# Optimization experiments

Hardware: AMD Instinct MI355X
Metric: run time of the kernel (lower is better)

The kernel has to match this reference:

```python
import jax, jax.numpy as jnp
import numpy as np

N_NODES = 100000
N_EDGES = 3200000
IN_CH = 256
OUT_CH = 1


def setup_inputs() -> dict:
    key = jax.random.key(0)
    ks = jax.random.split(key, 8)
    x = jax.random.normal(ks[0], (N_NODES, IN_CH), dtype=jnp.float32)
    edge_index = jax.random.randint(ks[1], (2, N_EDGES), 0, N_NODES, dtype=jnp.int64 if jax.config.jax_enable_x64 else jnp.int32)
    s_in = 1.0 / np.sqrt(IN_CH)
    Wq = jax.random.uniform(ks[2], (IN_CH, OUT_CH), jnp.float32, -s_in, s_in)
    bq = jax.random.uniform(ks[3], (OUT_CH,), jnp.float32, -s_in, s_in)
    Wk = jax.random.uniform(ks[4], (IN_CH, OUT_CH), jnp.float32, -s_in, s_in)
    bk = jax.random.uniform(ks[5], (OUT_CH,), jnp.float32, -s_in, s_in)
    Wv = jax.random.uniform(ks[6], (IN_CH, IN_CH), jnp.float32, -s_in, s_in)
    bv = jax.random.uniform(ks[7], (IN_CH,), jnp.float32, -s_in, s_in)
    return {"x": x, "edge_index": edge_index, "Wq": Wq, "bq": bq,
            "Wk": Wk, "bk": bk, "Wv": Wv, "bv": bv}


def reference(x, edge_index, Wq, bq, Wk, bk, Wv, bv):
    num_nodes = x.shape[0]
    q = x @ Wq + bq                       # [N, out_ch]
    k = x @ Wk + bk                       # [N, out_ch]
    v = x @ Wv + bv                       # [N, in_ch]
    row, col = edge_index[0], edge_index[1]
    # edge attention logits: gather + dot over out_ch
    att = jnp.sum(q[row] * k[col], axis=-1)          # [E]
    att = jax.nn.leaky_relu(att, negative_slope=0.2)
    att = jax.nn.softmax(att, axis=0)                # softmax over ALL edges (dim=0)
    # scatter-add edge attention to source nodes
    attention_weights = jax.ops.segment_sum(att, row, num_segments=num_nodes)  # [N]
    graph_emb = jnp.sum(attention_weights[:, None] * v, axis=0)                # [in_ch]
    return graph_emb, attention_weights
```

## Files before the change

kernel.cpp:

```cpp
#include <hip/hip_runtime.h>

#define N_NODES 100000
#define N_EDGES 3200000
#define CH 256

#define GRID_QK 1563
#define GRID_POOL 512
#define YCOPY 16

#define NR 8
#define RANGE 12500
#define SL 64
#define EPS 50000
#define HEPS 25000
#define GP 391

#define OFF_TOTAL 0
#define OFF_PTOT  16
#define OFF_YU16  528
#define OFF_Q     4624
#define OFF_K     104624
#define OFF_AWU   204624
#define OFF_PART  304624

__global__ __launch_bounds__(256) void k_qk(const float* __restrict__ x,
                                            const float* __restrict__ Wq,
                                            const float* __restrict__ bq,
                                            const float* __restrict__ Wk,
                                            const float* __restrict__ bk,
                                            float* __restrict__ q,
                                            float* __restrict__ k,
                                            float* __restrict__ yu16) {
    int t = threadIdx.x;
    if (blockIdx.x < 16) yu16[blockIdx.x * 256 + t] = 0.0f;
    int w = t >> 6, lane = t & 63;
    int g = lane >> 4, seg = lane & 15;
    float4 wq4[4], wk4[4];
    #pragma unroll
    for (int j = 0; j < 4; ++j) {
        wq4[j] = ((const float4*)Wq)[seg + 16 * j];
        wk4[j] = ((const float4*)Wk)[seg + 16 * j];
    }
    float bqs = bq[0], bks = bk[0];
    int base = blockIdx.x * 64 + w * 16 + g;
    #pragma unroll
    for (int i = 0; i < 4; ++i) {
        int n = base + i * 4;
        if (n < N_NODES) {
            const float4* xr = (const float4*)(x + (size_t)n * CH);
            float dq = 0.0f, dk = 0.0f;
            #pragma unroll
            for (int j = 0; j < 4; ++j) {
                float4 xv = xr[seg + 16 * j];
                dq = fmaf(xv.x, wq4[j].x, fmaf(xv.y, wq4[j].y,
                     fmaf(xv.z, wq4[j].z, fmaf(xv.w, wq4[j].w, dq))));
                dk = fmaf(xv.x, wk4[j].x, fmaf(xv.y, wk4[j].y,
                     fmaf(xv.z, wk4[j].z, fmaf(xv.w, wk4[j].w, dk))));
            }
            dq += __shfl_down(dq, 8); dq += __shfl_down(dq, 4);
            dq += __shfl_down(dq, 2); dq += __shfl_down(dq, 1);
            dk += __shfl_down(dk, 8); dk += __shfl_down(dk, 4);
            dk += __shfl_down(dk, 2); dk += __shfl_down(dk, 1);
            if (seg == 0) { q[n] = dq + bqs; k[n] = dk + bks; }
        }
    }
}

__global__ __launch_bounds__(1024) void k_acc(const int* __restrict__ ei,
                                              const float* __restrict__ q,
                                              const float* __restrict__ k,
                                              float* __restrict__ partial) {
    __shared__ float acc[RANGE];
    int t = threadIdx.x;
    int s = blockIdx.x >> 3, r = blockIdx.x & 7;
    for (int i = t; i < RANGE; i += 1024) acc[i] = 0.0f;
    __syncthreads();
    int r0 = r * RANGE;
    int e0 = s * EPS;
    for (int i = e0 + t; i < e0 + HEPS; i += 1024) {
        int rowA = ei[i];
        int rowB = ei[i + HEPS];
        unsigned offA = (unsigned)(rowA - r0);
        unsigned offB = (unsigned)(rowB - r0);
        if (offA < RANGE) {
            int col = ei[N_EDGES + i];
            float v = q[rowA] * k[col];
            v = (v >= 0.0f) ? v : 0.2f * v;
            atomicAdd(&acc[offA], __expf(v));
        }
        if (offB < RANGE) {
            int col = ei[N_EDGES + i + HEPS];
            float v = q[rowB] * k[col];
            v = (v >= 0.0f) ? v : 0.2f * v;
            atomicAdd(&acc[offB], __expf(v));
        }
    }
    __syncthreads();
    float* dst = partial + ((size_t)r * SL + s) * RANGE;
    for (int i = t; i < RANGE; i += 1024) dst[i] = acc[i];
}

__global__ __launch_bounds__(256) void k_fold(const float* __restrict__ partial,
                                              float* __restrict__ awu,
                                              float* __restrict__ ptot) {
    int t = threadIdx.x;
    int n = blockIdx.x * 256 + t;
    float s = 0.0f;
    if (n < N_NODES) {
        int r = n / RANGE, off = n % RANGE;
        const float* p = partial + (size_t)r * SL * RANGE + off;
        #pragma unroll 8
        for (int g = 0; g < SL; ++g) s += p[(size_t)g * RANGE];
        awu[n] = s;
    }
    float rsum = s;
    #pragma unroll
    for (int off = 32; off; off >>= 1) rsum += __shfl_down(rsum, off);
    __shared__ float sm[4];
    if ((t & 63) == 0) sm[t >> 6] = rsum;
    __syncthreads();
    if (t == 0) ptot[blockIdx.x] = sm[0] + sm[1] + sm[2] + sm[3];
}

__global__ __launch_bounds__(256) void k_pool(const float* __restrict__ x,
                                              const float* __restrict__ awu,
                                              const float* __restrict__ ptot,
                                              float* __restrict__ totalp,
                                              float* __restrict__ yu16,
                                              float* __restrict__ aw_out) {
    int t = threadIdx.x, s = t >> 6, g = t & 63;
    float ts = ptot[t] + ((t + 256 < GP) ? ptot[t + 256] : 0.0f);
    #pragma unroll
    for (int off = 32; off; off >>= 1) ts += __shfl_down(ts, off);
    __shared__ float sm[4];
    __shared__ float tot;
    if (g == 0) sm[s] = ts;
    __syncthreads();
    if (t == 0) {
        tot = sm[0] + sm[1] + sm[2] + sm[3];
        if (blockIdx.x == 0) totalp[0] = tot;
    }
    __syncthreads();
    float inv = 1.0f / tot;

    const float4* X4 = (const float4*)x;
    float4 acc = make_float4(0.f, 0.f, 0.f, 0.f);
    for (int base = blockIdx.x * 8; base < N_NODES; base += GRID_POOL * 8) {
        float a0 = awu[base + s];
        float a1 = awu[base + 4 + s];
        float4 x0 = X4[(size_t)(base + s) * 64 + g];
        float4 x1 = X4[(size_t)(base + 4 + s) * 64 + g];
        acc.x = fmaf(a0, x0.x, acc.x); acc.y = fmaf(a0, x0.y, acc.y);
        acc.z = fmaf(a0, x0.z, acc.z); acc.w = fmaf(a0, x0.w, acc.w);
        acc.x = fmaf(a1, x1.x, acc.x); acc.y = fmaf(a1, x1.y, acc.y);
        acc.z = fmaf(a1, x1.z, acc.z); acc.w = fmaf(a1, x1.w, acc.w);
    }
    __shared__ float4 tmp4[4][64];
    tmp4[s][g] = acc;
    __syncthreads();
    const float* tmp = (const float*)tmp4;
    float sum = tmp[0 * 256 + t] + tmp[1 * 256 + t] + tmp[2 * 256 + t] + tmp[3 * 256 + t];
    atomicAdd(&yu16[(blockIdx.x & (YCOPY - 1)) * 256 + t], sum);
    for (int i = blockIdx.x * 256 + t; i < N_NODES; i += GRID_POOL * 256)
        aw_out[i] = awu[i] * inv;
}

__global__ __launch_bounds__(256) void k_final(const float* __restrict__ yu16,
                                               const float* __restrict__ totalp,
                                               const float* __restrict__ Wv,
                                               const float* __restrict__ bv,
                                               float* __restrict__ out) {
    __shared__ float ysh[256];
    __shared__ float red[256];
    int t = threadIdx.x;
    float inv = 1.0f / totalp[0];
    float yv = 0.0f;
    #pragma unroll
    for (int j = 0; j < YCOPY; ++j) yv += yu16[j * 256 + t];
    ysh[t] = yv * inv;
    __syncthreads();
    int c = blockIdx.x * 32 + (t & 31), rg = t >> 5;
    float acc = 0.0f;
    #pragma unroll
    for (int j = 0; j < 32; ++j) {
        int kk = rg * 32 + j;
        acc = fmaf(ysh[kk], Wv[(size_t)kk * CH + c], acc);
    }
    red[t] = acc;
    __syncthreads();
    if (t < 32) {
        float sv = 0.0f;
        #pragma unroll
        for (int j = 0; j < 8; ++j) sv += red[j * 32 + t];
        out[blockIdx.x * 32 + t] = sv + bv[blockIdx.x * 32 + t];
    }
}

extern "C" void kernel_launch(void* const* d_in, const int* in_sizes, int n_in,
                              void* d_out, int out_size, void* d_ws, size_t ws_size,
                              hipStream_t stream) {
    const float* x  = (const float*)d_in[0];
    const int*   ei = (const int*)d_in[1];
    const float* Wq = (const float*)d_in[2];
    const float* bq = (const float*)d_in[3];
    const float* Wk = (const float*)d_in[4];
    const float* bk = (const float*)d_in[5];
    const float* Wv = (const float*)d_in[6];
    const float* bv = (const float*)d_in[7];
    float* out = (float*)d_out;
    float* ws  = (float*)d_ws;

    float* totalp  = ws + OFF_TOTAL;
    float* ptot    = ws + OFF_PTOT;
    float* yu16    = ws + OFF_YU16;
    float* q       = ws + OFF_Q;
    float* k       = ws + OFF_K;
    float* awu     = ws + OFF_AWU;
    float* partial = ws + OFF_PART;

    hipLaunchKernelGGL(k_qk, dim3(GRID_QK), dim3(256), 0, stream,
                       x, Wq, bq, Wk, bk, q, k, yu16);
    hipLaunchKernelGGL(k_acc, dim3(NR * SL), dim3(1024), 0, stream,
                       ei, q, k, partial);
    hipLaunchKernelGGL(k_fold, dim3(GP), dim3(256), 0, stream,
                       partial, awu, ptot);
    hipLaunchKernelGGL(k_pool, dim3(GRID_POOL), dim3(256), 0, stream,
                       x, awu, ptot, totalp, yu16, out + CH);
    hipLaunchKernelGGL(k_final, dim3(8), dim3(256), 0, stream,
                       yu16, totalp, Wv, bv, out);
}
```

Measured before the change: 260.9 us.

## Halve node-range passes in edge accumulation and vectorize row index loads

The edge-accumulation kernel now splits nodes into 4 ranges of 25000 instead of 8 ranges of 12500, held in 100KB of dynamic shared memory. Each edge's row index is therefore read by half as many blocks. Row indices are loaded as int4 so each thread handles four consecutive edges per iteration, and leaky-relu becomes a single fmaxf. The larger LDS footprint limits occupancy to fewer blocks per CU, and the total number of blocks drops from 512 to 256.

```diff
diff --git a/kernel.cpp b/kernel.cpp
--- a/kernel.cpp
+++ b/kernel.cpp
@@ -8,11 +8,11 @@
 #define GRID_POOL 512
 #define YCOPY 16
 
-#define NR 8
-#define RANGE 12500
+#define NR 4
+#define RANGE 25000
 #define SL 64
 #define EPS 50000
-#define HEPS 25000
+#define QEPS 12500
 #define GP 391
 
 #define OFF_TOTAL 0
@@ -70,29 +70,36 @@
                                               const float* __restrict__ q,
                                               const float* __restrict__ k,
                                               float* __restrict__ partial) {
-    __shared__ float acc[RANGE];
-    int t = threadIdx.x;
-    int s = blockIdx.x >> 3, r = blockIdx.x & 7;
+    extern __shared__ float acc[];
+    int t = threadIdx.x;
+    int s = blockIdx.x >> 2, r = blockIdx.x & 3;
     for (int i = t; i < RANGE; i += 1024) acc[i] = 0.0f;
     __syncthreads();
     int r0 = r * RANGE;
-    int e0 = s * EPS;
-    for (int i = e0 + t; i < e0 + HEPS; i += 1024) {
-        int rowA = ei[i];
-        int rowB = ei[i + HEPS];
-        unsigned offA = (unsigned)(rowA - r0);
-        unsigned offB = (unsigned)(rowB - r0);
-        if (offA < RANGE) {
-            int col = ei[N_EDGES + i];
-            float v = q[rowA] * k[col];
-            v = (v >= 0.0f) ? v : 0.2f * v;
-            atomicAdd(&acc[offA], __expf(v));
-        }
-        if (offB < RANGE) {
-            int col = ei[N_EDGES + i + HEPS];
-            float v = q[rowB] * k[col];
-            v = (v >= 0.0f) ? v : 0.2f * v;
-            atomicAdd(&acc[offB], __expf(v));
+    const int4* rows4 = (const int4*)ei;
+    int q0 = s * QEPS;
+    for (int i4 = q0 + t; i4 < q0 + QEPS; i4 += 1024) {
+        int4 rw = rows4[i4];
+        int eb = 4 * i4;
+        unsigned o0 = (unsigned)(rw.x - r0);
+        unsigned o1 = (unsigned)(rw.y - r0);
+        unsigned o2 = (unsigned)(rw.z - r0);
+        unsigned o3 = (unsigned)(rw.w - r0);
+        if (o0 < RANGE) {
+            float v = q[rw.x] * k[ei[N_EDGES + eb]];
+            atomicAdd(&acc[o0], __expf(fmaxf(v, 0.2f * v)));
+        }
+        if (o1 < RANGE) {
+            float v = q[rw.y] * k[ei[N_EDGES + eb + 1]];
+            atomicAdd(&acc[o1], __expf(fmaxf(v, 0.2f * v)));
+        }
+        if (o2 < RANGE) {
+            float v = q[rw.z] * k[ei[N_EDGES + eb + 2]];
+            atomicAdd(&acc[o2], __expf(fmaxf(v, 0.2f * v)));
+        }
+        if (o3 < RANGE) {
+            float v = q[rw.w] * k[ei[N_EDGES + eb + 3]];
+            atomicAdd(&acc[o3], __expf(fmaxf(v, 0.2f * v)));
         }
     }
     __syncthreads();
@@ -218,9 +225,17 @@
     float* awu     = ws + OFF_AWU;
     float* partial = ws + OFF_PART;
 
+    static bool lds_init = false;
+    if (!lds_init) {
+        (void)hipFuncSetAttribute((const void*)k_acc,
+                                  hipFuncAttributeMaxDynamicSharedMemorySize,
+                                  RANGE * 4);
+        lds_init = true;
+    }
+
     hipLaunchKernelGGL(k_qk, dim3(GRID_QK), dim3(256), 0, stream,
                        x, Wq, bq, Wk, bk, q, k, yu16);
-    hipLaunchKernelGGL(k_acc, dim3(NR * SL), dim3(1024), 0, stream,
+    hipLaunchKernelGGL(k_acc, dim3(NR * SL), dim3(1024), RANGE * 4, stream,
                        ei, q, k, partial);
     hipLaunchKernelGGL(k_fold, dim3(GP), dim3(256), 0, stream,
                        partial, awu, ptot);
```

After: 249.2 us. 1.05x faster.
